# Performance work log

Hardware: AMD Instinct MI355X
Metric: run time of the kernel (lower is better)

Reference implementation:

```python
import jax, jax.numpy as jnp
import numpy as np
import math
from fractions import Fraction

L_IN, L_OUT, STEP = 4, 4, 2  # symmetric=True -> step 2 (even l only)
_SQRT2 = math.sqrt(2.0)

# ---- real Wigner 3j symbols (e3nn convention: real SH basis, unit Frobenius norm) ----

def _fact(n):
    return Fraction(math.factorial(round(n)))

def _su2_cg(j1, m1, j2, m2, j3, m3):
    if m3 != m1 + m2:
        return 0.0
    vmin = int(max(-j1 + j2 + m3, -j1 + m1, 0))
    vmax = int(min(j2 + j3 + m1, j3 - j1 + j2, j3 + m3))
    C = float(((2 * j3 + 1) * Fraction(
        _fact(j3 + j1 - j2) * _fact(j3 - j1 + j2) * _fact(j1 + j2 - j3) * _fact(j3 + m3) * _fact(j3 - m3),
        _fact(j1 + j2 + j3 + 1) * _fact(j1 - m1) * _fact(j1 + m1) * _fact(j2 - m2) * _fact(j2 + m2))) ** 0.5)
    S = Fraction(0)
    for v in range(vmin, vmax + 1):
        S += (-1) ** (v + j2 + m2) * Fraction(
            _fact(j2 + j3 + m1 - v) * _fact(j1 - m1 + v),
            _fact(v) * _fact(j3 - j1 + j2 - v) * _fact(j3 + m3 - v) * _fact(v + j1 - j2 - m3))
    return C * float(S)

def _q_real_to_complex(l):
    q = np.zeros((2 * l + 1, 2 * l + 1), dtype=np.complex128)
    for m in range(-l, 0):
        q[l + m, l + abs(m)] = 1.0 / math.sqrt(2)
        q[l + m, l - abs(m)] = -1j / math.sqrt(2)
    q[l, l] = 1.0
    for m in range(1, l + 1):
        q[l + m, l + abs(m)] = (-1) ** m / math.sqrt(2)
        q[l + m, l - abs(m)] = 1j * (-1) ** m / math.sqrt(2)
    return ((-1j) ** l) * q

def _wigner_3j(l1, l2, l3):
    C = np.zeros((2 * l1 + 1, 2 * l2 + 1, 2 * l3 + 1))
    for m1 in range(-l1, l1 + 1):
        for m2 in range(-l2, l2 + 1):
            m3 = m1 + m2
            if abs(m3) <= l3:
                C[l1 + m1, l2 + m2, l3 + m3] = _su2_cg(l1, m1, l2, m2, l3, m3)
    Q1, Q2, Q3 = _q_real_to_complex(l1), _q_real_to_complex(l2), _q_real_to_complex(l3)
    C = np.einsum('ij,kl,mn,ikn->jlm', Q1, Q2, np.conj(Q3.T), C.astype(np.complex128))
    C = np.real(C)
    nrm = np.linalg.norm(C)
    return C / nrm if nrm > 0 else C

# ---- precompute (l, l1, l2) combinations and CG tables (constants) ----
_COMBOS = []
for _l in range(0, L_OUT + 1, STEP):
    for _l1 in range(0, L_IN + 1, STEP):
        for _l2 in range(0, L_IN + 1, STEP):
            if _l2 < _l1 or abs(_l2 - _l1) > _l or _l > _l1 + _l2:
                continue
            w = _wigner_3j(_l1, _l2, _l)                  # (2l1+1, 2l2+1, 2l+1)
            cg = np.transpose(w, (2, 1, 0))               # torch .T reverses all dims
            cg_r = cg.reshape(2 * _l + 1, 2 * _l1 + 1, 2 * _l2 + 1)  # raw reshape, as in source
            cg_l = np.transpose(cg_r, (0, 2, 1))
            if _l1 != _l2:
                cg_r = _SQRT2 * cg_r
                cg_l = _SQRT2 * cg_l
            _COMBOS.append((_l, _l1, _l2,
                            jnp.asarray(cg_r, jnp.float32),
                            jnp.asarray(cg_l, jnp.float32)))


def setup_inputs() -> dict:
    key = jax.random.key(0)
    k0, k2, k4, kf = jax.random.split(key, 4)
    N, A = 16, 16
    return {
        'rh0': jax.random.normal(k0, (N, A, A, A, 1, 1), dtype=jnp.float32),
        'rh2': jax.random.normal(k2, (N, A, A, A, 5, 5), dtype=jnp.float32),
        'rh4': jax.random.normal(k4, (N, A, A, A, 9, 9), dtype=jnp.float32),
        'feats': jax.random.normal(kf, (N, 64), dtype=jnp.float32),
    }


def reference(rh0, rh2, rh4, feats):
    rh = {0: rh0, 2: rh2, 4: rh4}
    n, a, b, c = rh0.shape[:4]
    rh_n = {}
    for (l, l1, l2, cg_r, cg_l) in _COMBOS:
        # x_r: [n,a,b,c, 2l+1, (2l1+1)*(2l2+1)]
        x_r = jnp.einsum('nabcij,klj->nabckli', rh[l2], cg_r)
        x_r = x_r.reshape(n, a, b, c, 2 * l + 1, -1)
        x_l = jnp.einsum('nabcji,klj->nabckil', rh[l1], cg_l)
        x_l = x_l.reshape(n, a, b, c, 2 * l + 1, -1)
        # batched small GEMM over the fused (2l1+1)(2l2+1) axis -> [n,a,b,c,2l+1,2l+1]
        x_a = jnp.einsum('nabcki,nabcji->nabckj', x_l, x_r)
        rh_n[l] = x_a if l not in rh_n else rh_n[l] + x_a
    # rotation-invariant features
    parts = [feats]
    for l in range(0, L_OUT + 1, STEP):
        n_l = 8.0 * math.pi ** 2 / (2 * l + 1)
        fl = jnp.sum(rh_n[l] ** 2, axis=(4, 5)).reshape(n, -1)  # [n, a*b*c]
        parts.append(n_l * fl)
    feats_out = jnp.concatenate(parts, axis=1)
    return rh_n[0], rh_n[2], rh_n[4], feats_out
```

## Files before the change

### kernel.cpp

```cpp
#include <hip/hip_runtime.h>
#include <math.h>
#include <utility>

#define DEV __device__ __forceinline__


constexpr double FC[14] = {1.,1.,2.,6.,24.,120.,720.,5040.,40320.,362880.,
                           3628800.,39916800.,479001600.,6227020800.};

constexpr double csqrt(double x) {
  if (x <= 0.0) return 0.0;
  double g = x > 1.0 ? x : 1.0;
  double p = 0.0;
  for (int i = 0; i < 64 && g != p; ++i) { p = g; g = 0.5 * (g + x / g); }
  return g;
}

constexpr int cimax(int a, int b) { return a > b ? a : b; }
constexpr int cimin(int a, int b) { return a < b ? a : b; }

constexpr double su2cg_c(int j1, int m1, int j2, int m2, int j3, int m3) {
  if (m3 != m1 + m2) return 0.0;
  int vmin = cimax(cimax(-j1 + j2 + m3, -j1 + m1), 0);
  int vmax = cimin(cimin(j2 + j3 + m1, j3 - j1 + j2), j3 + m3);
  if (vmax < vmin) return 0.0;
  double C = csqrt((2.0 * j3 + 1.0)
      * FC[j3 + j1 - j2] * FC[j3 - j1 + j2] * FC[j1 + j2 - j3]
      * FC[j3 + m3] * FC[j3 - m3]
      / (FC[j1 + j2 + j3 + 1] * FC[j1 - m1] * FC[j1 + m1]
         * FC[j2 - m2] * FC[j2 + m2]));
  double S = 0.0;
  for (int v = vmin; v <= vmax; ++v) {
    double term = FC[j2 + j3 + m1 - v] * FC[j1 - m1 + v]
        / (FC[v] * FC[j3 - j1 + j2 - v] * FC[j3 + m3 - v]
           * FC[v + j1 - j2 - m3]);
    S += ((v + j2 + m2) & 1) ? -term : term;
  }
  return C * S;
}

constexpr int nqcol(int l, int c, int* rows, double* vx, double* vy) {
  const double r2 = 0.70710678118654752440;
  double sg = (l % 4 == 2) ? -1.0 : 1.0;
  if (c == l) { rows[0] = l; vx[0] = sg; vy[0] = 0.0; return 1; }
  if (c > l) {
    int mm = c - l;
    double par = (mm & 1) ? -1.0 : 1.0;
    rows[0] = l - mm; vx[0] = sg * r2;       vy[0] = 0.0;
    rows[1] = l + mm; vx[1] = sg * par * r2; vy[1] = 0.0;
    return 2;
  }
  int mm = l - c;
  double par = (mm & 1) ? -1.0 : 1.0;
  rows[0] = l - mm; vx[0] = 0.0; vy[0] = -sg * r2;
  rows[1] = l + mm; vx[1] = 0.0; vy[1] = sg * par * r2;
  return 2;
}

constexpr int KCL [11] = {0,0,0, 2,2,2,2, 4,4,4,4};
constexpr int KCL1[11] = {0,2,4, 0,2,2,4, 0,2,2,4};
constexpr int KCL2[11] = {0,2,4, 2,2,4,4, 4,2,4,4};
constexpr int KOFF[11] = {0,1,26,107,132,257,482,887,968,1193,1598};

struct CCGT { double v[11][81]; };
constexpr CCGT make_ccg() {
  CCGT z = {};
  for (int c = 0; c < 11; ++c) {
    int l = KCL[c], l1 = KCL1[c], l2 = KCL2[c];
    int D1 = 2 * l1 + 1, D2 = 2 * l2 + 1;
    for (int a = 0; a < D1; ++a)
      for (int b = 0; b < D2; ++b) {
        int m1 = a - l1, m2 = b - l2, m3 = m1 + m2;
        z.v[c][a * D2 + b] =
            (m3 >= -l && m3 <= l) ? su2cg_c(l1, m1, l2, m2, l, m3) : 0.0;
      }
  }
  return z;
}
constexpr CCGT CCG = make_ccg();

struct CGTab { float r[2327]; float l[2327]; };
constexpr CGTab make_tables(const CCGT& cc) {
  CGTab t = {};
  for (int c = 0; c < 11; ++c) {
    int l = KCL[c], l1 = KCL1[c], l2 = KCL2[c];
    int D = 2 * l + 1, D1 = 2 * l1 + 1, D2 = 2 * l2 + 1;
    int n = D * D1 * D2, off = KOFF[c];
    double wbuf[729] = {};
    for (int e = 0; e < n; ++e) {
      int k = e % D; int ab = e / D; int b = ab % D2; int a = ab / D2;
      int r1[2] = {}, r2[2] = {}, r3[2] = {};
      double x1[2] = {}, y1[2] = {}, x2[2] = {}, y2[2] = {}, x3[2] = {}, y3[2] = {};
      int n1 = nqcol(l1, a, r1, x1, y1);
      int n2 = nqcol(l2, b, r2, x2, y2);
      int n3 = nqcol(l, k, r3, x3, y3);
      double s = 0.0;
      for (int i1 = 0; i1 < n1; ++i1)
        for (int i2 = 0; i2 < n2; ++i2) {
          double px = x1[i1] * x2[i2] - y1[i1] * y2[i2];
          double py = x1[i1] * y2[i2] + y1[i1] * x2[i2];
          int m12 = (r1[i1] - l1) + (r2[i2] - l2);
          for (int i3 = 0; i3 < n3; ++i3) {
            if (r3[i3] - l != m12) continue;
            s += (px * x3[i3] + py * y3[i3]) * cc.v[c][r1[i1] * D2 + r2[i2]];
          }
        }
      wbuf[e] = s;
    }
    double ss = 0.0;
    for (int e = 0; e < n; ++e) ss += wbuf[e] * wbuf[e];
    double inv = (l1 != l2 ? 1.41421356237309504880 : 1.0) / csqrt(ss);
    for (int o = 0; o < n; ++o) {
      int k = o / (D1 * D2), tt = o % (D1 * D2);
      int a = tt % D1, b = tt / D1;
      int x = tt / D2, y = tt % D2;
      double val = wbuf[(a * D2 + b) * D + k] * inv;
      t.r[off + o] = (float)val;
      t.l[off + k * (D1 * D2) + y * D1 + x] = (float)val;
    }
  }
  return t;
}
constexpr CGTab GT = make_tables(CCG);
__constant__ CGTab G = GT;

__global__ void setup_copy(float* __restrict__ ws,
                           const float* __restrict__ feats,
                           float* __restrict__ out) {
  int tid = threadIdx.x;
  if (blockIdx.x == 0) {
    for (int i = tid; i < 2327; i += 256) ws[i] = G.l[i];
  } else {
    for (int i = tid; i < 1024; i += 256) {
      int n = i >> 6, j = i & 63;
      out[7012352 + n * 12352 + j] = feats[i];
    }
  }
}


template<int OFF, int D1, int D2, int P, int K>
constexpr bool vr_row_nz() {
  for (int i = 0; i < D2; ++i)
    if (GT.r[OFF + K * D1 * D2 + P * D2 + i] != 0.0f) return true;
  return false;
}

template<int OFF, int D1, int D2, int P, int K, int I>
DEV void vr_step(const float* __restrict__ Brow, float& s) {
  constexpr float c = GT.r[OFF + K * D1 * D2 + P * D2 + I];
  if constexpr (c != 0.0f) s = fmaf(Brow[I], c, s);
}

template<int OFF, int D1, int D2, int P, int K, int... Is>
DEV float vr_k(const float* __restrict__ Brow, std::integer_sequence<int, Is...>) {
  float s = 0.f;
  (vr_step<OFF, D1, D2, P, K, Is>(Brow, s), ...);
  return s;
}

template<int OFF, int D, int D1, int D2, int P, int... Ks>
DEV void vr_all(const float* __restrict__ Brow, float* __restrict__ vr,
                std::integer_sequence<int, Ks...>) {
  ((vr[Ks] = vr_k<OFF, D1, D2, P, Ks>(Brow, std::make_integer_sequence<int, D2>{})), ...);
}

template<int OFF, int D, int D1, int D2, int P, int K1, int K2>
DEV void acc_one(const float* __restrict__ vl, const float* __restrict__ vr,
                 float* __restrict__ acc) {
  if constexpr (vr_row_nz<OFF, D1, D2, P, K2>())
    acc[K1 * D + K2] = fmaf(vl[K1], vr[K2], acc[K1 * D + K2]);
}

template<int OFF, int D, int D1, int D2, int P, int K1, int... K2s>
DEV void acc_row(const float* __restrict__ vl, const float* __restrict__ vr,
                 float* __restrict__ acc, std::integer_sequence<int, K2s...>) {
  (acc_one<OFF, D, D1, D2, P, K1, K2s>(vl, vr, acc), ...);
}

template<int OFF, int D, int D1, int D2, int P, int... K1s>
DEV void acc_all(const float* __restrict__ vl, const float* __restrict__ vr,
                 float* __restrict__ acc, std::integer_sequence<int, K1s...>) {
  (acc_row<OFF, D, D1, D2, P, K1s>(vl, vr, acc, std::make_integer_sequence<int, D>{}), ...);
}


template<int C, int D, int D1, int D2, int NP, int P0, int PP>
DEV void mp_one_p(const float* __restrict__ cglws, const float (&Acol)[NP][D1],
                  const float* __restrict__ Brow, int q, float* __restrict__ acc) {
  constexpr int OFF = KOFF[C];
  float vl[D];
  #pragma unroll
  for (int k = 0; k < D; ++k) {
    float s = 0.f;
    #pragma unroll
    for (int j = 0; j < D1; ++j)
      s = fmaf(Acol[PP][j], cglws[k * D1 * D2 + q * D1 + j], s);
    vl[k] = s;
  }
  float vr[D];
  vr_all<OFF, D, D1, D2, P0 + PP>(Brow, vr, std::make_integer_sequence<int, D>{});
  acc_all<OFF, D, D1, D2, P0 + PP>(vl, vr, acc, std::make_integer_sequence<int, D>{});
}

template<int C, int D, int D1, int D2, int NP, int P0, int... PPs>
DEV void mp_q_iter(const float* __restrict__ cglws, const float (&Acol)[NP][D1],
                   const float* __restrict__ Brow, int q, float* __restrict__ acc,
                   std::integer_sequence<int, PPs...>) {
  (mp_one_p<C, D, D1, D2, NP, P0, PPs>(cglws, Acol, Brow, q, acc), ...);
}

template<int C, int D, int D1, int D2, int P0, int NP>
DEV void combo_mp(const float* __restrict__ ws, const float* __restrict__ A,
                  const float* __restrict__ B, int lane, float* __restrict__ acc) {
  const float* cglws = ws + KOFF[C];
  float Acol[NP][D1];
  #pragma unroll
  for (int pp = 0; pp < NP; ++pp) {
    #pragma unroll
    for (int j = 0; j < D1; ++j)
      Acol[pp][j] = A[(j * D1 + P0 + pp) * 65 + lane];
  }
  #pragma unroll 1
  for (int q = 0; q < D2; ++q) {
    float Brow[D2];
    #pragma unroll
    for (int i = 0; i < D2; ++i) Brow[i] = B[(q * D2 + i) * 65 + lane];
    mp_q_iter<C, D, D1, D2, NP, P0>(cglws, Acol, Brow, q, acc,
                                    std::make_integer_sequence<int, NP>{});
  }
}

__global__ __launch_bounds__(256, 2)
void quad_main(const float* __restrict__ rh0, const float* __restrict__ rh2,
               const float* __restrict__ rh4, const float* __restrict__ ws,
               float* __restrict__ out) {
  __shared__ float lds[107 * 65];
  const int tid = threadIdx.x;
  const int lane = tid & 63;
  const int wave = tid >> 6;
  const int blk = blockIdx.x;
  const int site0 = blk * 64;

  if (tid < 64) lds[tid] = rh0[site0 + tid];
  for (int f = tid; f < 1600; f += 256) {
    int s = f / 25, e = f - s * 25;
    lds[(1 + e) * 65 + s] = rh2[site0 * 25 + f];
  }
  for (int f = tid; f < 5184; f += 256) {
    int s = f / 81, e = f - s * 81;
    lds[(26 + e) * 65 + s] = rh4[site0 * 81 + f];
  }
  __syncthreads();

  const float* r0 = lds;
  const float* r2l = lds + 65;
  const float* r4l = lds + 26 * 65;

  float acc0[1] = {0.f};
  float acc2[25], acc4[81];
  #pragma unroll
  for (int i = 0; i < 25; ++i) acc2[i] = 0.f;
  #pragma unroll
  for (int i = 0; i < 81; ++i) acc4[i] = 0.f;

  if (wave == 0) {
    combo_mp<10,9,9,9,0,2>(ws, r4l, r4l, lane, acc4);
    combo_mp<10,9,9,9,2,2>(ws, r4l, r4l, lane, acc4);
    combo_mp<10,9,9,9,4,2>(ws, r4l, r4l, lane, acc4);
  } else if (wave == 1) {
    combo_mp<6,5,9,9,0,3>(ws, r4l, r4l, lane, acc2);
    combo_mp<6,5,9,9,3,3>(ws, r4l, r4l, lane, acc2);
    combo_mp<6,5,9,9,6,3>(ws, r4l, r4l, lane, acc2);
    combo_mp<5,5,5,9,0,3>(ws, r2l, r4l, lane, acc2);
    combo_mp<5,5,5,9,3,2>(ws, r2l, r4l, lane, acc2);
  } else if (wave == 2) {
    combo_mp<9,9,5,9,0,2>(ws, r2l, r4l, lane, acc4);
    combo_mp<9,9,5,9,2,2>(ws, r2l, r4l, lane, acc4);
    combo_mp<9,9,5,9,4,1>(ws, r2l, r4l, lane, acc4);
    combo_mp<8,9,5,5,0,2>(ws, r2l, r2l, lane, acc4);
    combo_mp<8,9,5,5,2,2>(ws, r2l, r2l, lane, acc4);
  } else {
    combo_mp<10,9,9,9,6,1>(ws, r4l, r4l, lane, acc4);
    combo_mp<10,9,9,9,7,1>(ws, r4l, r4l, lane, acc4);
    combo_mp<10,9,9,9,8,1>(ws, r4l, r4l, lane, acc4);
    combo_mp<8,9,5,5,4,1>(ws, r2l, r2l, lane, acc4);
    combo_mp<7,9,1,9,0,1>(ws, r0, r4l, lane, acc4);
    combo_mp<4,5,5,5,0,1>(ws, r2l, r2l, lane, acc2);
    combo_mp<4,5,5,5,1,1>(ws, r2l, r2l, lane, acc2);
    combo_mp<4,5,5,5,2,1>(ws, r2l, r2l, lane, acc2);
    combo_mp<4,5,5,5,3,1>(ws, r2l, r2l, lane, acc2);
    combo_mp<4,5,5,5,4,1>(ws, r2l, r2l, lane, acc2);
    combo_mp<3,5,1,5,0,1>(ws, r0, r2l, lane, acc2);
    combo_mp<2,1,9,9,0,9>(ws, r4l, r4l, lane, acc0);
    combo_mp<1,1,5,5,0,5>(ws, r2l, r2l, lane, acc0);
    combo_mp<0,1,1,1,0,1>(ws, r0, r0, lane, acc0);
  }

  __syncthreads();
  if (wave == 0) {
    lds[lane] = acc0[0];
    #pragma unroll
    for (int e = 0; e < 25; ++e) lds[(1 + e) * 65 + lane] = acc2[e];
    #pragma unroll
    for (int e = 0; e < 81; ++e) lds[(26 + e) * 65 + lane] = acc4[e];
  }
  __syncthreads();
  if (wave == 1) {
    lds[lane] += acc0[0];
    #pragma unroll
    for (int e = 0; e < 25; ++e) lds[(1 + e) * 65 + lane] += acc2[e];
    #pragma unroll
    for (int e = 0; e < 81; ++e) lds[(26 + e) * 65 + lane] += acc4[e];
  }
  __syncthreads();
  if (wave == 2) {
    lds[lane] += acc0[0];
    #pragma unroll
    for (int e = 0; e < 25; ++e) lds[(1 + e) * 65 + lane] += acc2[e];
    #pragma unroll
    for (int e = 0; e < 81; ++e) lds[(26 + e) * 65 + lane] += acc4[e];
  }
  __syncthreads();
  if (wave == 3) {
    lds[lane] += acc0[0];
    #pragma unroll
    for (int e = 0; e < 25; ++e) lds[(1 + e) * 65 + lane] += acc2[e];
    #pragma unroll
    for (int e = 0; e < 81; ++e) lds[(26 + e) * 65 + lane] += acc4[e];
  }
  __syncthreads();

  if (tid < 64) out[site0 + tid] = lds[tid];
  for (int f = tid; f < 1600; f += 256) {
    int s = f / 25, e = f - s * 25;
    out[65536 + blk * 1600 + f] = lds[(1 + e) * 65 + s];
  }
  for (int f = tid; f < 5184; f += 256) {
    int s = f / 81, e = f - s * 81;
    out[1703936 + blk * 5184 + f] = lds[(26 + e) * 65 + s];
  }

  if (tid < 64) {
    int site = site0 + tid;
    int nn = site >> 12, abc = site & 4095;
    float v0 = lds[tid];
    float f0 = v0 * v0;
    float s2 = 0.f;
    #pragma unroll
    for (int e = 0; e < 25; ++e) { float v = lds[(1 + e) * 65 + tid]; s2 = fmaf(v, v, s2); }
    float s4 = 0.f;
    #pragma unroll
    for (int e = 0; e < 81; ++e) { float v = lds[(26 + e) * 65 + tid]; s4 = fmaf(v, v, s4); }
    const float PI8 = 78.95683520871486f;
    int base = 7012352 + nn * 12352 + 64;
    out[base + abc] = PI8 * f0;
    out[base + 4096 + abc] = (PI8 / 5.f) * s2;
    out[base + 8192 + abc] = (PI8 / 9.f) * s4;
  }
}

extern "C" void kernel_launch(void* const* d_in, const int* in_sizes, int n_in,
                              void* d_out, int out_size, void* d_ws, size_t ws_size,
                              hipStream_t stream) {
  const float* rh0 = (const float*)d_in[0];
  const float* rh2 = (const float*)d_in[1];
  const float* rh4 = (const float*)d_in[2];
  const float* feats = (const float*)d_in[3];
  float* out = (float*)d_out;
  float* ws = (float*)d_ws;
  setup_copy<<<2, 256, 0, stream>>>(ws, feats, out);
  quad_main<<<1024, 256, 0, stream>>>(rh0, rh2, rh4, ws, out);
}
```

Measured before the change: 164.1 us.

## Split combo work across six waves and reduce partials with LDS atomics

Blocks grow from four to six waves, and the CG combo pieces are rebalanced so four waves own only the l=4 accumulators and two waves own the l=0/l=2 accumulators. This cuts per-wave register use and the critical-path work per wave. The serial four-stage LDS reduction becomes one store followed by a single round of LDS atomicAdd, which removes two barriers. In exchange, launch bounds rise to 384 threads with 3 blocks per CU, which tightens the register budget, and LDS float atomics add contention among three waves.

```diff
diff --git a/kernel.cpp b/kernel.cpp
--- a/kernel.cpp
+++ b/kernel.cpp
@@ -231,7 +231,7 @@
   }
 }
 
-__global__ __launch_bounds__(256, 2)
+__global__ __launch_bounds__(384, 3)
 void quad_main(const float* __restrict__ rh0, const float* __restrict__ rh2,
                const float* __restrict__ rh4, const float* __restrict__ ws,
                float* __restrict__ out) {
@@ -243,11 +243,11 @@
   const int site0 = blk * 64;
 
   if (tid < 64) lds[tid] = rh0[site0 + tid];
-  for (int f = tid; f < 1600; f += 256) {
+  for (int f = tid; f < 1600; f += 384) {
     int s = f / 25, e = f - s * 25;
     lds[(1 + e) * 65 + s] = rh2[site0 * 25 + f];
   }
-  for (int f = tid; f < 5184; f += 256) {
+  for (int f = tid; f < 5184; f += 384) {
     int s = f / 81, e = f - s * 81;
     lds[(26 + e) * 65 + s] = rh4[site0 * 81 + f];
   }
@@ -257,86 +257,76 @@
   const float* r2l = lds + 65;
   const float* r4l = lds + 26 * 65;
 
-  float acc0[1] = {0.f};
-  float acc2[25], acc4[81];
-  #pragma unroll
-  for (int i = 0; i < 25; ++i) acc2[i] = 0.f;
-  #pragma unroll
-  for (int i = 0; i < 81; ++i) acc4[i] = 0.f;
+  float acc0[1], acc2[25], acc4[81];
+  if (wave <= 3) {
+    #pragma unroll
+    for (int i = 0; i < 81; ++i) acc4[i] = 0.f;
+  } else {
+    acc0[0] = 0.f;
+    #pragma unroll
+    for (int i = 0; i < 25; ++i) acc2[i] = 0.f;
+  }
 
   if (wave == 0) {
     combo_mp<10,9,9,9,0,2>(ws, r4l, r4l, lane, acc4);
     combo_mp<10,9,9,9,2,2>(ws, r4l, r4l, lane, acc4);
+  } else if (wave == 1) {
     combo_mp<10,9,9,9,4,2>(ws, r4l, r4l, lane, acc4);
-  } else if (wave == 1) {
+    combo_mp<10,9,9,9,6,2>(ws, r4l, r4l, lane, acc4);
+  } else if (wave == 2) {
+    combo_mp<10,9,9,9,8,1>(ws, r4l, r4l, lane, acc4);
+    combo_mp<9,9,5,9,0,2>(ws, r2l, r4l, lane, acc4);
+    combo_mp<9,9,5,9,2,2>(ws, r2l, r4l, lane, acc4);
+  } else if (wave == 3) {
+    combo_mp<9,9,5,9,4,1>(ws, r2l, r4l, lane, acc4);
+    combo_mp<8,9,5,5,0,2>(ws, r2l, r2l, lane, acc4);
+    combo_mp<8,9,5,5,2,2>(ws, r2l, r2l, lane, acc4);
+    combo_mp<8,9,5,5,4,1>(ws, r2l, r2l, lane, acc4);
+    combo_mp<7,9,1,9,0,1>(ws, r0, r4l, lane, acc4);
+  } else if (wave == 4) {
     combo_mp<6,5,9,9,0,3>(ws, r4l, r4l, lane, acc2);
     combo_mp<6,5,9,9,3,3>(ws, r4l, r4l, lane, acc2);
     combo_mp<6,5,9,9,6,3>(ws, r4l, r4l, lane, acc2);
+    combo_mp<3,5,1,5,0,1>(ws, r0, r2l, lane, acc2);
+    combo_mp<1,1,5,5,0,5>(ws, r2l, r2l, lane, acc0);
+    combo_mp<0,1,1,1,0,1>(ws, r0, r0, lane, acc0);
+  } else {
     combo_mp<5,5,5,9,0,3>(ws, r2l, r4l, lane, acc2);
     combo_mp<5,5,5,9,3,2>(ws, r2l, r4l, lane, acc2);
-  } else if (wave == 2) {
-    combo_mp<9,9,5,9,0,2>(ws, r2l, r4l, lane, acc4);
-    combo_mp<9,9,5,9,2,2>(ws, r2l, r4l, lane, acc4);
-    combo_mp<9,9,5,9,4,1>(ws, r2l, r4l, lane, acc4);
-    combo_mp<8,9,5,5,0,2>(ws, r2l, r2l, lane, acc4);
-    combo_mp<8,9,5,5,2,2>(ws, r2l, r2l, lane, acc4);
-  } else {
-    combo_mp<10,9,9,9,6,1>(ws, r4l, r4l, lane, acc4);
-    combo_mp<10,9,9,9,7,1>(ws, r4l, r4l, lane, acc4);
-    combo_mp<10,9,9,9,8,1>(ws, r4l, r4l, lane, acc4);
-    combo_mp<8,9,5,5,4,1>(ws, r2l, r2l, lane, acc4);
-    combo_mp<7,9,1,9,0,1>(ws, r0, r4l, lane, acc4);
-    combo_mp<4,5,5,5,0,1>(ws, r2l, r2l, lane, acc2);
-    combo_mp<4,5,5,5,1,1>(ws, r2l, r2l, lane, acc2);
-    combo_mp<4,5,5,5,2,1>(ws, r2l, r2l, lane, acc2);
-    combo_mp<4,5,5,5,3,1>(ws, r2l, r2l, lane, acc2);
+    combo_mp<4,5,5,5,0,2>(ws, r2l, r2l, lane, acc2);
+    combo_mp<4,5,5,5,2,2>(ws, r2l, r2l, lane, acc2);
     combo_mp<4,5,5,5,4,1>(ws, r2l, r2l, lane, acc2);
-    combo_mp<3,5,1,5,0,1>(ws, r0, r2l, lane, acc2);
-    combo_mp<2,1,9,9,0,9>(ws, r4l, r4l, lane, acc0);
-    combo_mp<1,1,5,5,0,5>(ws, r2l, r2l, lane, acc0);
-    combo_mp<0,1,1,1,0,1>(ws, r0, r0, lane, acc0);
+    combo_mp<2,1,9,9,0,3>(ws, r4l, r4l, lane, acc0);
+    combo_mp<2,1,9,9,3,3>(ws, r4l, r4l, lane, acc0);
+    combo_mp<2,1,9,9,6,3>(ws, r4l, r4l, lane, acc0);
   }
 
   __syncthreads();
   if (wave == 0) {
+    #pragma unroll
+    for (int e = 0; e < 81; ++e) lds[(26 + e) * 65 + lane] = acc4[e];
+  } else if (wave == 4) {
     lds[lane] = acc0[0];
     #pragma unroll
     for (int e = 0; e < 25; ++e) lds[(1 + e) * 65 + lane] = acc2[e];
-    #pragma unroll
-    for (int e = 0; e < 81; ++e) lds[(26 + e) * 65 + lane] = acc4[e];
   }
   __syncthreads();
-  if (wave == 1) {
-    lds[lane] += acc0[0];
-    #pragma unroll
-    for (int e = 0; e < 25; ++e) lds[(1 + e) * 65 + lane] += acc2[e];
-    #pragma unroll
-    for (int e = 0; e < 81; ++e) lds[(26 + e) * 65 + lane] += acc4[e];
+  if (wave >= 1 && wave <= 3) {
+    #pragma unroll
+    for (int e = 0; e < 81; ++e) atomicAdd(&lds[(26 + e) * 65 + lane], acc4[e]);
+  } else if (wave == 5) {
+    atomicAdd(&lds[lane], acc0[0]);
+    #pragma unroll
+    for (int e = 0; e < 25; ++e) atomicAdd(&lds[(1 + e) * 65 + lane], acc2[e]);
   }
   __syncthreads();
-  if (wave == 2) {
-    lds[lane] += acc0[0];
-    #pragma unroll
-    for (int e = 0; e < 25; ++e) lds[(1 + e) * 65 + lane] += acc2[e];
-    #pragma unroll
-    for (int e = 0; e < 81; ++e) lds[(26 + e) * 65 + lane] += acc4[e];
-  }
-  __syncthreads();
-  if (wave == 3) {
-    lds[lane] += acc0[0];
-    #pragma unroll
-    for (int e = 0; e < 25; ++e) lds[(1 + e) * 65 + lane] += acc2[e];
-    #pragma unroll
-    for (int e = 0; e < 81; ++e) lds[(26 + e) * 65 + lane] += acc4[e];
-  }
-  __syncthreads();
 
   if (tid < 64) out[site0 + tid] = lds[tid];
-  for (int f = tid; f < 1600; f += 256) {
+  for (int f = tid; f < 1600; f += 384) {
     int s = f / 25, e = f - s * 25;
     out[65536 + blk * 1600 + f] = lds[(1 + e) * 65 + s];
   }
-  for (int f = tid; f < 5184; f += 256) {
+  for (int f = tid; f < 5184; f += 384) {
     int s = f / 81, e = f - s * 81;
     out[1703936 + blk * 5184 + f] = lds[(26 + e) * 65 + s];
   }
@@ -370,5 +360,5 @@
   float* out = (float*)d_out;
   float* ws = (float*)d_ws;
   setup_copy<<<2, 256, 0, stream>>>(ws, feats, out);
-  quad_main<<<1024, 256, 0, stream>>>(rh0, rh2, rh4, ws, out);
-}
+  quad_main<<<1024, 384, 0, stream>>>(rh0, rh2, rh4, ws, out);
+}
```

New measurement: 277.0 us. 68.8% more time.
